# Kernel tuning notes

Hardware: AMD Instinct MI355X
Metric: run time of the kernel (lower is better)

## Reference

```python
import jax, jax.numpy as jnp
import numpy as np

HEADS = 8
DIM_HEAD = 8
UP = 64  # nn.Upsample(scale_factor=64) on the score map
DN = ('NCHW', 'OIHW', 'NCHW')


def setup_inputs() -> dict:
    key = jax.random.key(0)
    ks = jax.random.split(key, 6)
    dim, inner = 64, HEADS * DIM_HEAD
    f = jax.random.normal(ks[0], (1, dim, 64, 64), dtype=jnp.float32)
    w_qkv = jax.random.normal(ks[1], (3 * inner, dim, 1, 1), dtype=jnp.float32) * 0.05
    wq = jax.random.normal(ks[2], (inner, inner, 11, 11), dtype=jnp.float32) * 0.02
    bq = jax.random.normal(ks[3], (inner,), dtype=jnp.float32) * 0.02
    wk = jax.random.normal(ks[4], (inner, inner, 11, 11), dtype=jnp.float32) * 0.02
    bk = jax.random.normal(ks[5], (inner,), dtype=jnp.float32) * 0.02
    return {'f': f, 'w_qkv': w_qkv, 'wq': wq, 'bq': bq, 'wk': wk, 'bk': bk}


def _down_conv(x, w, b):
    # Conv2d(inner, inner, (11,11), stride (8,8), padding 2) + exact GELU
    y = jax.lax.conv_general_dilated(x, w, (8, 8), ((2, 2), (2, 2)), dimension_numbers=DN)
    return jax.nn.gelu(y + b[None, :, None, None], approximate=False)


def _split_heads(t):
    # 'b (h c) x y -> b h c (x y)'
    bb, cc, x, y = t.shape
    return t.reshape(bb, HEADS, cc // HEADS, x * y)


def reference(f, w_qkv, wq, bq, wk, bk):
    b, _, H, W = f.shape
    scale = DIM_HEAD ** -0.5
    # 1x1 conv qkv projection, no bias
    qkv = jax.lax.conv_general_dilated(f, w_qkv, (1, 1), ((0, 0), (0, 0)), dimension_numbers=DN)
    q, k, v = jnp.split(qkv, 3, axis=1)
    q = _split_heads(_down_conv(q, wq, bq)) * scale  # [b,h,c,n_low]
    k = _split_heads(_down_conv(k, wk, bk))          # [b,h,c,n_low]
    v = _split_heads(v)                              # [b,h,c,HW]
    dots = jnp.einsum('bhci,bhcj->bhij', q, k)       # [b,h,n_low,n_low]
    # nearest-neighbor upsample by 64 on both score dims -> [b,h,HW,HW]
    dots = jnp.repeat(jnp.repeat(dots, UP, axis=2), UP, axis=3)
    attn = jax.nn.softmax(dots, axis=-1)
    fmap = jnp.einsum('bhij,bhcj->bhci', attn, v)    # [b,h,c,HW]
    return fmap.reshape(b, HEADS * DIM_HEAD, H, W)
```

## Files before the change

### kernel.cpp

```cpp
#include <hip/hip_runtime.h>

#define SCALE 0.35355339059327379f
#define RSQRT2 0.70710678118654752f

#define PL      4624
#define QP_OFF  0
#define KP_OFF  (64*PL)
#define PART_OFF (2*64*PL)
#define VP_OFF  (PART_OFF + 256*4096)
#define QD_OFF  (VP_OFF + 4*4096)
#define KD_OFF  (QD_OFF + 4096)
#define VR_OFF  (KD_OFF + 4096)

__global__ __launch_bounds__(384) void k1(const float* __restrict__ f,
                                          const float* __restrict__ w_qkv,
                                          float* __restrict__ ws)
{
    __shared__ float sm[14656];
    const int b = blockIdx.x, t = threadIdx.x;
    const int x = b >> 1, yh = b & 1;
    float* wt = sm;
    float* fl = sm + 12352;

    {
        float* plane = ws + (yh ? KP_OFF : QP_OFF) + x*PL;
        for (int j = t; j < 528; j += 384) {
            int idx;
            if (j < 272) {
                const int rp = j / 68, c = j % 68;
                const int row = (rp < 2) ? rp : rp + 64;
                idx = row*68 + c;
            } else {
                const int jj = j - 272;
                const int cp = jj >> 6, r2 = (jj & 63) + 2;
                const int col = (cp < 2) ? cp : cp + 64;
                idx = r2*68 + col;
            }
            plane[idx] = 0.f;
        }
    }
    #pragma unroll
    for (int j = 0; j < 8; ++j) {
        const int idx = t + 384*j;
        const float4 v = *(const float4*)(w_qkv + 4*idx);
        const int oc = idx >> 4, ic0 = (4*idx) & 63;
        wt[(ic0+0)*193 + oc] = v.x;
        wt[(ic0+1)*193 + oc] = v.y;
        wt[(ic0+2)*193 + oc] = v.z;
        wt[(ic0+3)*193 + oc] = v.w;
    }
    for (int i = t; i < 512; i += 384) {
        const int ic = i >> 3, p = i & 7;
        *(float4*)&fl[ic*36 + p*4] = *(const float4*)(f + ic*4096 + x*64 + yh*32 + p*4);
    }
    __syncthreads();

    const int w = t >> 6, lane = t & 63;
    const int type = w >> 1, yoct = w & 1;
    float acc[16];
    #pragma unroll
    for (int j = 0; j < 16; ++j) acc[j] = 0.f;
    #pragma unroll 4
    for (int ic = 0; ic < 64; ++ic) {
        const float wv = wt[ic*193 + type*64 + lane];
        const float4 p0 = *(const float4*)&fl[ic*36 + yoct*16];
        const float4 p1 = *(const float4*)&fl[ic*36 + yoct*16 + 4];
        const float4 p2 = *(const float4*)&fl[ic*36 + yoct*16 + 8];
        const float4 p3 = *(const float4*)&fl[ic*36 + yoct*16 + 12];
        acc[0]  = fmaf(wv, p0.x, acc[0]);  acc[1]  = fmaf(wv, p0.y, acc[1]);
        acc[2]  = fmaf(wv, p0.z, acc[2]);  acc[3]  = fmaf(wv, p0.w, acc[3]);
        acc[4]  = fmaf(wv, p1.x, acc[4]);  acc[5]  = fmaf(wv, p1.y, acc[5]);
        acc[6]  = fmaf(wv, p1.z, acc[6]);  acc[7]  = fmaf(wv, p1.w, acc[7]);
        acc[8]  = fmaf(wv, p2.x, acc[8]);  acc[9]  = fmaf(wv, p2.y, acc[9]);
        acc[10] = fmaf(wv, p2.z, acc[10]); acc[11] = fmaf(wv, p2.w, acc[11]);
        acc[12] = fmaf(wv, p3.x, acc[12]); acc[13] = fmaf(wv, p3.y, acc[13]);
        acc[14] = fmaf(wv, p3.z, acc[14]); acc[15] = fmaf(wv, p3.w, acc[15]);
    }
    if (type < 2) {
        float* plane = ws + (type ? KP_OFF : QP_OFF) + lane*PL;
        const int base = (x + 2)*68 + yh*32 + yoct*16 + 2;
        #pragma unroll
        for (int j = 0; j < 8; ++j)
            *(float2*)(plane + base + 2*j) = make_float2(acc[2*j], acc[2*j+1]);
    } else {
        float s = 0.f;
        #pragma unroll
        for (int j = 0; j < 16; ++j) s += acc[j];
        (ws + VP_OFF)[(yh*2 + yoct)*4096 + x*64 + lane] = s * 0.015625f;
    }
}

__global__ __launch_bounds__(512) void k2(const float* __restrict__ ws_qP,
                                          const float* __restrict__ ws_kP,
                                          const float* __restrict__ wq,
                                          const float* __restrict__ wk,
                                          float* __restrict__ part)
{
    const int b = blockIdx.x, t = threadIdx.x;
    const int type = b >> 7, ic = (b >> 1) & 63, khh = b & 1;
    const int kh0 = khh ? 6 : 0, nkh = khh ? 5 : 6;
    const float* plane = (type ? ws_kP : ws_qP) + ic*PL;
    const float* wsrc  = (type ? wk : wq) + ic*121 + kh0*11;
    const int lane = t & 63;
    const int oc0 = __builtin_amdgcn_readfirstlane(t >> 6) * 8;
    const int ox = lane >> 3, oy = lane & 7;

    float acc[8] = {0.f,0.f,0.f,0.f,0.f,0.f,0.f,0.f};
    #pragma unroll
    for (int khl = 0; khl < 6; ++khl) {
        if (khl < nkh) {
            const int xp = ox*8 + kh0 + khl;
            const float* prow = plane + xp*68 + oy*8;
            const float4 r0 = *(const float4*)(prow);
            const float4 r1 = *(const float4*)(prow + 4);
            const float4 r2 = *(const float4*)(prow + 8);
            const float pr[12] = {r0.x,r0.y,r0.z,r0.w, r1.x,r1.y,r1.z,r1.w,
                                  r2.x,r2.y,r2.z,r2.w};
            const float* wrow = wsrc + khl*11;
            #pragma unroll
            for (int kw = 0; kw < 11; ++kw) {
                const float pv = pr[kw];
                #pragma unroll
                for (int j = 0; j < 8; ++j) {
                    const float wgt = wrow[(oc0 + j)*7744 + kw];
                    acc[j] = fmaf(wgt, pv, acc[j]);
                }
            }
        }
    }
    float* pp = part + (size_t)b*4096 + lane;
    #pragma unroll
    for (int j = 0; j < 8; ++j) pp[(oc0 + j)*64] = acc[j];
}

__global__ __launch_bounds__(256) void k2r(const float* __restrict__ part,
                                           const float* __restrict__ Vpart,
                                           const float* __restrict__ bq,
                                           const float* __restrict__ bk,
                                           float* __restrict__ qd,
                                           float* __restrict__ kd,
                                           float* __restrict__ Vrow)
{
    __shared__ float red[4][64];
    const int b = blockIdx.x, t = threadIdx.x;
    const int type = b >> 6, oc = b & 63;
    const int il = t & 63, q4 = t >> 6;
    float s = 0.f;
    #pragma unroll 8
    for (int p = q4*32; p < q4*32 + 32; ++p)
        s += part[(size_t)(type*128 + p)*4096 + oc*64 + il];
    red[q4][il] = s;
    if (type == 0 && q4 == 1) {
        float v = 0.f;
        #pragma unroll
        for (int p = 0; p < 4; ++p) v += Vpart[p*4096 + oc*64 + il];
        Vrow[oc*64 + il] = v;
    }
    __syncthreads();
    if (t < 64) {
        const float tot = red[0][t] + red[1][t] + red[2][t] + red[3][t];
        const float v = tot + (type ? bk[oc] : bq[oc]);
        (type ? kd : qd)[oc*64 + t] = 0.5f*v*(1.0f + erff(v*RSQRT2));
    }
}

__global__ __launch_bounds__(512) void k3(const float* __restrict__ qd,
                                          const float* __restrict__ kd,
                                          const float* __restrict__ VrowG,
                                          float* __restrict__ out)
{
    __shared__ float vrow[64*65];
    const int x = blockIdx.x, t = threadIdx.x;
    for (int idx = t; idx < 4096; idx += 512) {
        const int jl = idx >> 6, ch = idx & 63;
        vrow[ch*65 + jl] = VrowG[idx];
    }
    __syncthreads();
    const int h = t >> 6, lane = t & 63;
    float d = 0.f;
    #pragma unroll
    for (int c = 0; c < 8; ++c)
        d = fmaf(qd[(h*8 + c)*64 + x], kd[(h*8 + c)*64 + lane], d);
    d *= SCALE;
    float m = d;
    #pragma unroll
    for (int mm = 1; mm < 64; mm <<= 1) m = fmaxf(m, __shfl_xor(m, mm, 64));
    const float e = __expf(d - m);
    float ssum = e;
    #pragma unroll
    for (int mm = 1; mm < 64; mm <<= 1) ssum += __shfl_xor(ssum, mm, 64);
    const float p = e / ssum;
    #pragma unroll
    for (int c = 0; c < 8; ++c) {
        float r = p * vrow[(h*8 + c)*65 + lane];
        #pragma unroll
        for (int mm = 1; mm < 64; mm <<= 1) r += __shfl_xor(r, mm, 64);
        out[(h*8 + c)*4096 + x*64 + lane] = r;
    }
}

extern "C" void kernel_launch(void* const* d_in, const int* in_sizes, int n_in,
                              void* d_out, int out_size, void* d_ws, size_t ws_size,
                              hipStream_t stream) {
    const float* f     = (const float*)d_in[0];
    const float* w_qkv = (const float*)d_in[1];
    const float* wq    = (const float*)d_in[2];
    const float* bq    = (const float*)d_in[3];
    const float* wk    = (const float*)d_in[4];
    const float* bk    = (const float*)d_in[5];
    float* out = (float*)d_out;
    float* ws  = (float*)d_ws;

    k1<<<128, 384, 0, stream>>>(f, w_qkv, ws);
    k2<<<256, 512, 0, stream>>>(ws + QP_OFF, ws + KP_OFF, wq, wk, ws + PART_OFF);
    k2r<<<128, 256, 0, stream>>>(ws + PART_OFF, ws + VP_OFF, bq, bk,
                                 ws + QD_OFF, ws + KD_OFF, ws + VR_OFF);
    k3<<<64, 512, 0, stream>>>(ws + QD_OFF, ws + KD_OFF, ws + VR_OFF, out);
}
```

Measured before the change: 27.81 us.

## Replace partial-sum reduction kernel with atomics and fuse bias+GELU into attention kernel

The k2 conv blocks now atomically accumulate their per-input-channel partials directly into q/k accumulators, which k1 zeroes, instead of writing 256 partial tiles to workspace. The separate k2r reduction kernel is removed. Its bias, GELU and V-partial summation move into k3, where each block recomputes GELU for all of k and its own q column. This saves a launch and the partial-buffer traffic, at the cost of atomic contention (128 adds per address) and redundant GELU work across 64 blocks.

```diff
diff --git a/kernel.cpp b/kernel.cpp
--- a/kernel.cpp
+++ b/kernel.cpp
@@ -6,11 +6,9 @@
 #define PL      4624
 #define QP_OFF  0
 #define KP_OFF  (64*PL)
-#define PART_OFF (2*64*PL)
-#define VP_OFF  (PART_OFF + 256*4096)
-#define QD_OFF  (VP_OFF + 4*4096)
-#define KD_OFF  (QD_OFF + 4096)
-#define VR_OFF  (KD_OFF + 4096)
+#define VP_OFF  (2*64*PL)
+#define QA_OFF  (VP_OFF + 4*4096)
+#define KA_OFF  (QA_OFF + 4096)
 
 __global__ __launch_bounds__(384) void k1(const float* __restrict__ f,
                                           const float* __restrict__ w_qkv,
@@ -21,6 +19,8 @@
     const int x = b >> 1, yh = b & 1;
     float* wt = sm;
     float* fl = sm + 12352;
+
+    if (t < 64) (ws + QA_OFF)[b*64 + t] = 0.f;
 
     {
         float* plane = ws + (yh ? KP_OFF : QP_OFF) + x*PL;
@@ -94,7 +94,8 @@
                                           const float* __restrict__ ws_kP,
                                           const float* __restrict__ wq,
                                           const float* __restrict__ wk,
-                                          float* __restrict__ part)
+                                          float* __restrict__ qa,
+                                          float* __restrict__ ka)
 {
     const int b = blockIdx.x, t = threadIdx.x;
     const int type = b >> 7, ic = (b >> 1) & 63, khh = b & 1;
@@ -128,59 +129,45 @@
             }
         }
     }
-    float* pp = part + (size_t)b*4096 + lane;
-    #pragma unroll
-    for (int j = 0; j < 8; ++j) pp[(oc0 + j)*64] = acc[j];
-}
-
-__global__ __launch_bounds__(256) void k2r(const float* __restrict__ part,
-                                           const float* __restrict__ Vpart,
-                                           const float* __restrict__ bq,
-                                           const float* __restrict__ bk,
-                                           float* __restrict__ qd,
-                                           float* __restrict__ kd,
-                                           float* __restrict__ Vrow)
-{
-    __shared__ float red[4][64];
-    const int b = blockIdx.x, t = threadIdx.x;
-    const int type = b >> 6, oc = b & 63;
-    const int il = t & 63, q4 = t >> 6;
-    float s = 0.f;
-    #pragma unroll 8
-    for (int p = q4*32; p < q4*32 + 32; ++p)
-        s += part[(size_t)(type*128 + p)*4096 + oc*64 + il];
-    red[q4][il] = s;
-    if (type == 0 && q4 == 1) {
-        float v = 0.f;
-        #pragma unroll
-        for (int p = 0; p < 4; ++p) v += Vpart[p*4096 + oc*64 + il];
-        Vrow[oc*64 + il] = v;
-    }
-    __syncthreads();
-    if (t < 64) {
-        const float tot = red[0][t] + red[1][t] + red[2][t] + red[3][t];
-        const float v = tot + (type ? bk[oc] : bq[oc]);
-        (type ? kd : qd)[oc*64 + t] = 0.5f*v*(1.0f + erff(v*RSQRT2));
-    }
-}
-
-__global__ __launch_bounds__(512) void k3(const float* __restrict__ qd,
-                                          const float* __restrict__ kd,
-                                          const float* __restrict__ VrowG,
+    float* ab = (type ? ka : qa) + lane;
+    #pragma unroll
+    for (int j = 0; j < 8; ++j)
+        atomicAdd(ab + (oc0 + j)*64, acc[j]);
+}
+
+__global__ __launch_bounds__(512) void k3(const float* __restrict__ qa,
+                                          const float* __restrict__ ka,
+                                          const float* __restrict__ Vpart,
+                                          const float* __restrict__ bq,
+                                          const float* __restrict__ bk,
                                           float* __restrict__ out)
 {
     __shared__ float vrow[64*65];
+    __shared__ float kg[4096];
     const int x = blockIdx.x, t = threadIdx.x;
     for (int idx = t; idx < 4096; idx += 512) {
         const int jl = idx >> 6, ch = idx & 63;
-        vrow[ch*65 + jl] = VrowG[idx];
+        float s = 0.f;
+        #pragma unroll
+        for (int p = 0; p < 4; ++p) s += Vpart[p*4096 + jl*64 + ch];
+        vrow[ch*65 + jl] = s;
+        const int oc = jl, il = ch;
+        const float v = ka[oc*64 + il] + bk[oc];
+        kg[oc*64 + il] = 0.5f*v*(1.0f + erff(v*RSQRT2));
     }
     __syncthreads();
     const int h = t >> 6, lane = t & 63;
+    float qg[8];
+    #pragma unroll
+    for (int c = 0; c < 8; ++c) {
+        const int oc = h*8 + c;
+        const float v = qa[oc*64 + x] + bq[oc];
+        qg[c] = 0.5f*v*(1.0f + erff(v*RSQRT2));
+    }
     float d = 0.f;
     #pragma unroll
     for (int c = 0; c < 8; ++c)
-        d = fmaf(qd[(h*8 + c)*64 + x], kd[(h*8 + c)*64 + lane], d);
+        d = fmaf(qg[c], kg[(h*8 + c)*64 + lane], d);
     d *= SCALE;
     float m = d;
     #pragma unroll
@@ -212,8 +199,8 @@
     float* ws  = (float*)d_ws;
 
     k1<<<128, 384, 0, stream>>>(f, w_qkv, ws);
-    k2<<<256, 512, 0, stream>>>(ws + QP_OFF, ws + KP_OFF, wq, wk, ws + PART_OFF);
-    k2r<<<128, 256, 0, stream>>>(ws + PART_OFF, ws + VP_OFF, bq, bk,
-                                 ws + QD_OFF, ws + KD_OFF, ws + VR_OFF);
-    k3<<<64, 512, 0, stream>>>(ws + QD_OFF, ws + KD_OFF, ws + VR_OFF, out);
-}
+    k2<<<256, 512, 0, stream>>>(ws + QP_OFF, ws + KP_OFF, wq, wk,
+                                ws + QA_OFF, ws + KA_OFF);
+    k3<<<64, 512, 0, stream>>>(ws + QA_OFF, ws + KA_OFF, ws + VP_OFF,
+                               bq, bk, out);
+}
```

Result: slower. 30.78 us (+10.7%).

## Fuse split-K reduction and GELU into attention kernel, dropping k2r launch

Applied to the files above, without the earlier changes.

Removes the separate reduction kernel and has each attention block reduce the partial conv sums for its head's K (all 64 positions), its 8 query rows and V, then apply bias and GELU locally. The work is re-partitioned so each block covers one head and 8 query rows. This saves a kernel launch and a global round trip for qd/kd/Vrow. In exchange, each block's K reduction (128 strided loads per thread) is repeated across the 8 blocks of a head, adding redundant global reads.

```diff
diff --git a/kernel.cpp b/kernel.cpp
--- a/kernel.cpp
+++ b/kernel.cpp
@@ -8,9 +8,6 @@
 #define KP_OFF  (64*PL)
 #define PART_OFF (2*64*PL)
 #define VP_OFF  (PART_OFF + 256*4096)
-#define QD_OFF  (VP_OFF + 4*4096)
-#define KD_OFF  (QD_OFF + 4096)
-#define VR_OFF  (KD_OFF + 4096)
 
 __global__ __launch_bounds__(384) void k1(const float* __restrict__ f,
                                           const float* __restrict__ w_qkv,
@@ -133,54 +130,52 @@
     for (int j = 0; j < 8; ++j) pp[(oc0 + j)*64] = acc[j];
 }
 
-__global__ __launch_bounds__(256) void k2r(const float* __restrict__ part,
-                                           const float* __restrict__ Vpart,
-                                           const float* __restrict__ bq,
-                                           const float* __restrict__ bk,
-                                           float* __restrict__ qd,
-                                           float* __restrict__ kd,
-                                           float* __restrict__ Vrow)
-{
-    __shared__ float red[4][64];
-    const int b = blockIdx.x, t = threadIdx.x;
-    const int type = b >> 6, oc = b & 63;
-    const int il = t & 63, q4 = t >> 6;
-    float s = 0.f;
-    #pragma unroll 8
-    for (int p = q4*32; p < q4*32 + 32; ++p)
-        s += part[(size_t)(type*128 + p)*4096 + oc*64 + il];
-    red[q4][il] = s;
-    if (type == 0 && q4 == 1) {
-        float v = 0.f;
-        #pragma unroll
-        for (int p = 0; p < 4; ++p) v += Vpart[p*4096 + oc*64 + il];
-        Vrow[oc*64 + il] = v;
-    }
-    __syncthreads();
-    if (t < 64) {
-        const float tot = red[0][t] + red[1][t] + red[2][t] + red[3][t];
-        const float v = tot + (type ? bk[oc] : bq[oc]);
-        (type ? kd : qd)[oc*64 + t] = 0.5f*v*(1.0f + erff(v*RSQRT2));
-    }
-}
-
-__global__ __launch_bounds__(512) void k3(const float* __restrict__ qd,
-                                          const float* __restrict__ kd,
-                                          const float* __restrict__ VrowG,
+__global__ __launch_bounds__(512) void k3(const float* __restrict__ part,
+                                          const float* __restrict__ Vpart,
+                                          const float* __restrict__ bq,
+                                          const float* __restrict__ bk,
                                           float* __restrict__ out)
 {
-    __shared__ float vrow[64*65];
-    const int x = blockIdx.x, t = threadIdx.x;
-    for (int idx = t; idx < 4096; idx += 512) {
-        const int jl = idx >> 6, ch = idx & 63;
-        vrow[ch*65 + jl] = VrowG[idx];
+    __shared__ float kg[512];
+    __shared__ float vr[512];
+    __shared__ float qg[64];
+    const int b = blockIdx.x, t = threadIdx.x;
+    const int h = b >> 3, xo = b & 7;
+    const int c = t >> 6, jl = t & 63;
+    const int oc = h*8 + c;
+
+    {
+        float s = 0.f;
+        const float* pp = part + (size_t)128*4096 + oc*64 + jl;
+        #pragma unroll 8
+        for (int p = 0; p < 128; ++p) s += pp[(size_t)p*4096];
+        const float v = s + bk[oc];
+        kg[c*64 + jl] = 0.5f*v*(1.0f + erff(v*RSQRT2));
+    }
+    {
+        float s = 0.f;
+        #pragma unroll
+        for (int p = 0; p < 4; ++p) s += Vpart[p*4096 + jl*64 + oc];
+        vr[c*64 + jl] = s;
+    }
+    if (t < 64) {
+        const int cc = t >> 3, xl = t & 7;
+        const int qoc = h*8 + cc;
+        const int il = xo*8 + xl;
+        float s = 0.f;
+        const float* pp = part + qoc*64 + il;
+        #pragma unroll 8
+        for (int p = 0; p < 128; ++p) s += pp[(size_t)p*4096];
+        const float v = s + bq[qoc];
+        qg[cc*8 + xl] = 0.5f*v*(1.0f + erff(v*RSQRT2));
     }
     __syncthreads();
-    const int h = t >> 6, lane = t & 63;
+
+    const int w = t >> 6, lane = t & 63;
     float d = 0.f;
     #pragma unroll
-    for (int c = 0; c < 8; ++c)
-        d = fmaf(qd[(h*8 + c)*64 + x], kd[(h*8 + c)*64 + lane], d);
+    for (int cc = 0; cc < 8; ++cc)
+        d = fmaf(qg[cc*8 + w], kg[cc*64 + lane], d);
     d *= SCALE;
     float m = d;
     #pragma unroll
@@ -190,12 +185,13 @@
     #pragma unroll
     for (int mm = 1; mm < 64; mm <<= 1) ssum += __shfl_xor(ssum, mm, 64);
     const float p = e / ssum;
-    #pragma unroll
-    for (int c = 0; c < 8; ++c) {
-        float r = p * vrow[(h*8 + c)*65 + lane];
+    const int x = xo*8 + w;
+    #pragma unroll
+    for (int cc = 0; cc < 8; ++cc) {
+        float r = p * vr[cc*64 + lane];
         #pragma unroll
         for (int mm = 1; mm < 64; mm <<= 1) r += __shfl_xor(r, mm, 64);
-        out[(h*8 + c)*4096 + x*64 + lane] = r;
+        out[(h*8 + cc)*4096 + x*64 + lane] = r;
     }
 }
 
@@ -213,7 +209,5 @@
 
     k1<<<128, 384, 0, stream>>>(f, w_qkv, ws);
     k2<<<256, 512, 0, stream>>>(ws + QP_OFF, ws + KP_OFF, wq, wk, ws + PART_OFF);
-    k2r<<<128, 256, 0, stream>>>(ws + PART_OFF, ws + VP_OFF, bq, bk,
-                                 ws + QD_OFF, ws + KD_OFF, ws + VR_OFF);
-    k3<<<64, 512, 0, stream>>>(ws + QD_OFF, ws + KD_OFF, ws + VR_OFF, out);
-}
+    k3<<<64, 512, 0, stream>>>(ws + PART_OFF, ws + VP_OFF, bq, bk, out);
+}
```

Measured after the change: 44.81 us. 61.1% more time.
